# Kernel tuning notes

Measured on AMD Instinct MI355X. Metric: run time of the kernel, lower is better.

Reference implementation:

```python
import jax, jax.numpy as jnp
import numpy as np

DIM = 64
N_ENTITY = 1000000
N_RELATION = 32
L = 2
B = 4096
K = 64


def setup_inputs() -> dict:
    key = jax.random.key(0)
    ks = jax.random.split(key, 24)
    s = 0.05
    d = DIM
    inp = {
        "items": jax.random.randint(ks[0], (B,), 0, N_ENTITY),
        "heads": jax.random.randint(ks[1], (L, B, K), 0, N_ENTITY),
        "relations": jax.random.randint(ks[2], (L, B, K), 0, N_RELATION),
        "tails": jax.random.randint(ks[3], (L, B, K), 0, N_ENTITY),
        # learned parameters
        "embedding": jax.random.normal(ks[4], (N_ENTITY, d), jnp.float32) * s,
        "transformer": jax.random.normal(ks[5], (N_RELATION, d), jnp.float32) * s,
        "attn_w": jax.random.normal(ks[6], (1, 3 * d), jnp.float32) * s,
        "attn_b": jax.random.normal(ks[7], (1,), jnp.float32) * s,
        "W_ih": jax.random.normal(ks[8], (d, d), jnp.float32) * s,
        "W_hh": jax.random.normal(ks[9], (d, d), jnp.float32) * s,
        "b_ih": jax.random.normal(ks[10], (d,), jnp.float32) * s,
        "b_hh": jax.random.normal(ks[11], (d,), jnp.float32) * s,
        "l1_w": jax.random.normal(ks[12], (d, 2 * d), jnp.float32) * s,
        "l1_b": jax.random.normal(ks[13], (d,), jnp.float32) * s,
        "l2_w": jax.random.normal(ks[14], (d, d), jnp.float32) * s,
        "l2_b": jax.random.normal(ks[15], (d,), jnp.float32) * s,
        "l3_w": jax.random.normal(ks[16], (d, d), jnp.float32) * s,
        "l3_b": jax.random.normal(ks[17], (d,), jnp.float32) * s,
        "lin_w": jax.random.normal(ks[18], (1, 2 * d), jnp.float32) * s,
        "lin_b": jax.random.normal(ks[19], (1,), jnp.float32) * s,
    }
    return inp


def _ncfg_forward(embedding, transformer, attn_w, attn_b, W_ih, W_hh, b_ih, b_hh,
                  l1_w, l1_b, l2_w, l2_b, l3_w, l3_b, lin_w, lin_b,
                  items, heads, relations, tails):
    o_sum = jnp.zeros((B, DIM), embedding.dtype)
    for l in range(L):
        h = embedding[heads[l]]          # [B, K, d]
        r = transformer[relations[l]]    # [B, K, d]
        tl = embedding[tails[l]]         # [B, K, d]
        hRt = jnp.concatenate([h, r, tl], axis=-1)                  # [B, K, 3d]
        pi = jax.nn.sigmoid(hRt @ attn_w.T + attn_b)                # [B, K, 1]
        pi = jax.nn.softmax(pi, axis=1)                             # softmax over neighbors
        # 2-step tanh RNN over seq (head, tail), h0 = 0
        h1 = jnp.tanh(h @ W_ih.T + b_ih + b_hh)                     # [B, K, d]
        h2 = jnp.tanh(tl @ W_ih.T + b_ih + h1 @ W_hh.T + b_hh)      # [B, K, d]
        o_sum = o_sum + (pi * h2).sum(axis=1)                       # [B, d]
    user_emb = o_sum
    item_emb = embedding[items]                                     # [B, d]
    # NCF head (dropout in eval mode = identity)
    ui = jnp.concatenate([user_emb, item_emb], axis=-1)             # [B, 2d]
    y = jax.nn.relu(ui @ l1_w.T + l1_b)
    y = jax.nn.relu(y @ l2_w.T + l2_b)
    y1 = jax.nn.sigmoid(y @ l3_w.T + l3_b)
    y2 = user_emb * item_emb
    out = jax.nn.sigmoid(jnp.concatenate([y1, y2], axis=-1) @ lin_w.T + lin_b)
    return out[:, 0]  # squeeze -> [B]


def reference(items, heads, relations, tails, embedding, transformer, attn_w, attn_b,
              W_ih, W_hh, b_ih, b_hh, l1_w, l1_b, l2_w, l2_b, l3_w, l3_b, lin_w, lin_b):
    return _ncfg_forward(embedding, transformer, attn_w, attn_b, W_ih, W_hh, b_ih, b_hh,
                         l1_w, l1_b, l2_w, l2_b, l3_w, l3_b, lin_w, lin_b,
                         items, heads, relations, tails)
```

## Files before the change

### kernel.cpp

```cpp
#include <hip/hip_runtime.h>
#include <hip/hip_bf16.h>
#include <cstdint>
#include <cstddef>

#define B_SZ 4096

typedef __attribute__((ext_vector_type(4))) float f32x4;
typedef __attribute__((ext_vector_type(8))) short sv8;
typedef __attribute__((ext_vector_type(8))) __bf16 bfv8;

__device__ __align__(16) short g_wf[2][8][64][8];
__device__ __align__(16) short g_af[2][2][64][8];
__device__ float g_bsum[64];
__device__ float g_reldot[32];

static __device__ __forceinline__ short f2bf(float x) {
  union { float f; unsigned u; } v; v.f = x;
  unsigned r = v.u + 0x7fffu + ((v.u >> 16) & 1u);
  return (short)(r >> 16);
}

static __device__ __forceinline__ f32x4 MFMA(sv8 a, sv8 b, f32x4 c) {
  return __builtin_amdgcn_mfma_f32_16x16x32_bf16(
      __builtin_bit_cast(bfv8, a), __builtin_bit_cast(bfv8, b), c, 0, 0, 0);
}

static __device__ __forceinline__ float fast_sigmoid(float x) {
  return __builtin_amdgcn_rcpf(1.f + __expf(-x));
}
static __device__ __forceinline__ float fast_tanh(float x) {
  const float e = __expf(2.f * x);
  return 1.f - 2.f * __builtin_amdgcn_rcpf(e + 1.f);
}
static __device__ __forceinline__ sv8 pack8(f32x4 a, f32x4 b) {
  sv8 f;
  f[0] = f2bf(a.x); f[1] = f2bf(a.y); f[2] = f2bf(a.z); f[3] = f2bf(a.w);
  f[4] = f2bf(b.x); f[5] = f2bf(b.y); f[6] = f2bf(b.z); f[7] = f2bf(b.w);
  return f;
}

__global__ __launch_bounds__(256) void ncfg_prep(
    const float* __restrict__ W_ih, const float* __restrict__ W_hh,
    const float* __restrict__ b_ih, const float* __restrict__ b_hh,
    const float* __restrict__ trf, const float* __restrict__ attn_w) {
  const int t = threadIdx.x;
  for (int q = t; q < 1024; q += 256) {
    const int m = q >> 9, f = (q >> 6) & 7, ln = q & 63;
    const int nt = f >> 1, kh = f & 1, fr = ln & 15, fg = ln >> 4;
    const float* W = m ? W_hh : W_ih;
    const float* src = W + (nt * 16 + fr) * 64 + kh * 32 + fg * 8;
    short* dst = &g_wf[m][f][ln][0];
    #pragma unroll
    for (int j = 0; j < 8; ++j) dst[j] = f2bf(src[j]);
  }
  {
    const int a = t >> 7, kh = (t >> 6) & 1, ln = t & 63;
    const int n = ln & 15, kf = ln >> 4;
    short* dst = &g_af[a][kh][ln][0];
    #pragma unroll
    for (int j = 0; j < 8; ++j)
      dst[j] = (n == 0) ? f2bf(attn_w[a * 128 + kh * 32 + kf * 8 + j]) : (short)0;
  }
  if (t < 64) g_bsum[t] = b_ih[t] + b_hh[t];
  if (t < 32) {
    float s = 0.f;
    #pragma unroll 8
    for (int c = 0; c < 64; ++c) s += trf[t * 64 + c] * attn_w[64 + c];
    g_reldot[t] = s;
  }
}

__global__ __launch_bounds__(256, 3) void ncfg_neigh(
    const int* __restrict__ heads, const int* __restrict__ rels,
    const int* __restrict__ tails, const float* __restrict__ emb,
    const float* __restrict__ attn_b, float* __restrict__ opart) {
  const int t = threadIdx.x;
  const int lane = t & 63;
  const int w = t >> 6;
  const int fr = lane & 15;
  const int fg = lane >> 4;
  const int c0 = fg * 8;

  __shared__ __align__(16) short h1s[4][16 * 72];
  __shared__ float ow[4][64];
  __shared__ float sew[4];

  const size_t ibase = (size_t)blockIdx.x * 64;

  const int hi = heads[ibase + (w << 4) + fr];
  const int ti = tails[ibase + (w << 4) + fr];
  const int ri = rels[ibase + (w << 4) + fr];

  const float* hr = emb + (size_t)hi * 64;
  const float* tr = emb + (size_t)ti * 64;
  const f32x4 h0 = *(const f32x4*)(hr + c0);
  const f32x4 h1 = *(const f32x4*)(hr + c0 + 4);
  const f32x4 h2 = *(const f32x4*)(hr + 32 + c0);
  const f32x4 h3 = *(const f32x4*)(hr + 32 + c0 + 4);
  const f32x4 t0 = *(const f32x4*)(tr + c0);
  const f32x4 t1 = *(const f32x4*)(tr + c0 + 4);
  const f32x4 t2 = *(const f32x4*)(tr + 32 + c0);
  const f32x4 t3 = *(const f32x4*)(tr + 32 + c0 + 4);

  sv8 wih[8], abf[4];
  #pragma unroll
  for (int f = 0; f < 8; ++f) wih[f] = *(const sv8*)&g_wf[0][f][lane][0];
  abf[0] = *(const sv8*)&g_af[0][0][lane][0];
  abf[1] = *(const sv8*)&g_af[0][1][lane][0];
  abf[2] = *(const sv8*)&g_af[1][0][lane][0];
  abf[3] = *(const sv8*)&g_af[1][1][lane][0];
  float bsum[4];
  #pragma unroll
  for (int nt = 0; nt < 4; ++nt) bsum[nt] = g_bsum[nt * 16 + fr];
  const float ab0 = attn_b[0];

  const sv8 ha0 = pack8(h0, h1), ha1 = pack8(h2, h3);
  const sv8 ta0 = pack8(t0, t1), ta1 = pack8(t2, t3);

  const f32x4 zz = {0.f, 0.f, 0.f, 0.f};

  f32x4 accl = zz;
  accl = MFMA(ha0, abf[0], accl);
  accl = MFMA(ha1, abf[1], accl);
  accl = MFMA(ta0, abf[2], accl);
  accl = MFMA(ta1, abf[3], accl);

  f32x4 ev;
  #pragma unroll
  for (int r = 0; r < 4; ++r) {
    const float lg = __shfl(accl[r], fg << 4);
    const int rr = __shfl(ri, (fg << 2) + r);
    ev[r] = __expf(fast_sigmoid(lg + g_reldot[rr] + ab0));
  }
  float se = ev.x + ev.y + ev.z + ev.w;
  se += __shfl_xor(se, 16);
  se += __shfl_xor(se, 32);

  f32x4 acc[4] = {zz, zz, zz, zz};
  #pragma unroll
  for (int nt = 0; nt < 4; ++nt) acc[nt] = MFMA(ha0, wih[nt * 2], acc[nt]);
  #pragma unroll
  for (int nt = 0; nt < 4; ++nt) acc[nt] = MFMA(ha1, wih[nt * 2 + 1], acc[nt]);

  sv8 whh[8];
  #pragma unroll
  for (int f = 0; f < 8; ++f) whh[f] = *(const sv8*)&g_wf[1][f][lane][0];

  #pragma unroll
  for (int nt = 0; nt < 4; ++nt)
    #pragma unroll
    for (int r = 0; r < 4; ++r)
      h1s[w][((fg << 2) + r) * 72 + nt * 16 + fr] =
          f2bf(fast_tanh(acc[nt][r] + bsum[nt]));

  f32x4 acc2[4] = {zz, zz, zz, zz};
  #pragma unroll
  for (int nt = 0; nt < 4; ++nt) acc2[nt] = MFMA(ta0, wih[nt * 2], acc2[nt]);
  #pragma unroll
  for (int nt = 0; nt < 4; ++nt) acc2[nt] = MFMA(ta1, wih[nt * 2 + 1], acc2[nt]);
  const sv8 a1 = *(const sv8*)&h1s[w][fr * 72 + c0];
  const sv8 a2 = *(const sv8*)&h1s[w][fr * 72 + 32 + c0];
  #pragma unroll
  for (int nt = 0; nt < 4; ++nt) acc2[nt] = MFMA(a1, whh[nt * 2], acc2[nt]);
  #pragma unroll
  for (int nt = 0; nt < 4; ++nt) acc2[nt] = MFMA(a2, whh[nt * 2 + 1], acc2[nt]);

  #pragma unroll
  for (int nt = 0; nt < 4; ++nt) {
    float s = ev.x * fast_tanh(acc2[nt][0] + bsum[nt]) +
              ev.y * fast_tanh(acc2[nt][1] + bsum[nt]) +
              ev.z * fast_tanh(acc2[nt][2] + bsum[nt]) +
              ev.w * fast_tanh(acc2[nt][3] + bsum[nt]);
    s += __shfl_xor(s, 16);
    s += __shfl_xor(s, 32);
    if (fg == 0) ow[w][nt * 16 + fr] = s;
  }
  if (lane == 0) sew[w] = se;

  __syncthreads();

  if (w == 0) {
    const float o = ow[0][lane] + ow[1][lane] + ow[2][lane] + ow[3][lane];
    const float st = sew[0] + sew[1] + sew[2] + sew[3];
    opart[ibase + lane] = o * __builtin_amdgcn_rcpf(st);
  }
}

__global__ __launch_bounds__(256) void ncfg_head(
    const float* __restrict__ opart, const float* __restrict__ emb,
    const int* __restrict__ items, const float* __restrict__ l1_w,
    const float* __restrict__ l1_b, const float* __restrict__ l2_w,
    const float* __restrict__ l2_b, const float* __restrict__ l3_w,
    const float* __restrict__ l3_b, const float* __restrict__ lin_w,
    const float* __restrict__ lin_b, float* __restrict__ out) {
  const int wv = threadIdx.x >> 6;
  const int i = threadIdx.x & 63;
  const int b = blockIdx.x * 4 + wv;

  __shared__ float ui[4][128];
  __shared__ float yy[4][64];

  const float ue = opart[(size_t)b * 64 + i] +
                   opart[((size_t)B_SZ + b) * 64 + i];
  const float ie = emb[(size_t)items[b] * 64 + i];
  ui[wv][i] = ue;
  ui[wv][64 + i] = ie;
  __syncthreads();

  float acc = l1_b[i];
  {
    const float* wr = l1_w + i * 128;
    #pragma unroll
    for (int j = 0; j < 128; j += 4) {
      const f32x4 wvv = *(const f32x4*)(wr + j);
      const f32x4 uv = *(const f32x4*)&ui[wv][j];
      acc += wvv.x * uv.x + wvv.y * uv.y + wvv.z * uv.z + wvv.w * uv.w;
    }
  }
  float y = fmaxf(acc, 0.f);
  yy[wv][i] = y;
  __syncthreads();

  acc = l2_b[i];
  {
    const float* wr = l2_w + i * 64;
    #pragma unroll
    for (int j = 0; j < 64; j += 4) {
      const f32x4 wvv = *(const f32x4*)(wr + j);
      const f32x4 uv = *(const f32x4*)&yy[wv][j];
      acc += wvv.x * uv.x + wvv.y * uv.y + wvv.z * uv.z + wvv.w * uv.w;
    }
  }
  y = fmaxf(acc, 0.f);
  __syncthreads();
  yy[wv][i] = y;
  __syncthreads();

  acc = l3_b[i];
  {
    const float* wr = l3_w + i * 64;
    #pragma unroll
    for (int j = 0; j < 64; j += 4) {
      const f32x4 wvv = *(const f32x4*)(wr + j);
      const f32x4 uv = *(const f32x4*)&yy[wv][j];
      acc += wvv.x * uv.x + wvv.y * uv.y + wvv.z * uv.z + wvv.w * uv.w;
    }
  }
  const float y1 = fast_sigmoid(acc);
  const float y2 = ue * ie;

  float part = y1 * lin_w[i] + y2 * lin_w[64 + i];
  #pragma unroll
  for (int m = 1; m < 64; m <<= 1) part += __shfl_xor(part, m);
  if (i == 0) out[b] = fast_sigmoid(part + lin_b[0]);
}

extern "C" void kernel_launch(void* const* d_in, const int* in_sizes, int n_in,
                              void* d_out, int out_size, void* d_ws,
                              size_t ws_size, hipStream_t stream) {
  (void)in_sizes; (void)n_in; (void)out_size; (void)ws_size;
  const int* items = (const int*)d_in[0];
  const int* heads = (const int*)d_in[1];
  const int* rels = (const int*)d_in[2];
  const int* tails = (const int*)d_in[3];
  const float* emb = (const float*)d_in[4];
  const float* trf = (const float*)d_in[5];
  const float* attn_w = (const float*)d_in[6];
  const float* attn_b = (const float*)d_in[7];
  const float* W_ih = (const float*)d_in[8];
  const float* W_hh = (const float*)d_in[9];
  const float* b_ih = (const float*)d_in[10];
  const float* b_hh = (const float*)d_in[11];
  const float* l1_w = (const float*)d_in[12];
  const float* l1_b = (const float*)d_in[13];
  const float* l2_w = (const float*)d_in[14];
  const float* l2_b = (const float*)d_in[15];
  const float* l3_w = (const float*)d_in[16];
  const float* l3_b = (const float*)d_in[17];
  const float* lin_w = (const float*)d_in[18];
  const float* lin_b = (const float*)d_in[19];
  float* out = (float*)d_out;
  float* opart = (float*)d_ws;

  ncfg_prep<<<dim3(1), dim3(256), 0, stream>>>(W_ih, W_hh, b_ih, b_hh, trf,
                                               attn_w);
  ncfg_neigh<<<dim3(2 * B_SZ), dim3(256), 0, stream>>>(
      heads, rels, tails, emb, attn_b, opart);
  ncfg_head<<<dim3(B_SZ / 4), dim3(256), 0, stream>>>(
      opart, emb, items, l1_w, l1_b, l2_w, l2_b, l3_w, l3_b, lin_w, lin_b,
      out);
}
```

Before: 95.69 us.

## Process a whole item per wave with LDS-staged weights and prefetched gathers

Each wave now handles all 64 neighbours of one (layer, batch) item in four chunks of 16, instead of each block splitting one item across four waves. Weight fragments are staged once per block into LDS rather than held in registers from global memory. The next chunk's embedding rows are prefetched while the current chunk computes. The per-item reduction stays within the wave, so the cross-wave shared-memory reduction and end barrier go away, the grid shrinks by 4x, and the occupancy hint rises to 4. The costs are extra LDS reads for every MFMA operand, a barrier after staging, and more serial work per wave, which means fewer waves in flight to hide gather latency.

```diff
diff --git a/kernel.cpp b/kernel.cpp
--- a/kernel.cpp
+++ b/kernel.cpp
@@ -70,7 +70,7 @@
   }
 }
 
-__global__ __launch_bounds__(256, 3) void ncfg_neigh(
+__global__ __launch_bounds__(256, 4) void ncfg_neigh(
     const int* __restrict__ heads, const int* __restrict__ rels,
     const int* __restrict__ tails, const float* __restrict__ emb,
     const float* __restrict__ attn_b, float* __restrict__ opart) {
@@ -81,109 +81,133 @@
   const int fg = lane >> 4;
   const int c0 = fg * 8;
 
+  __shared__ __align__(16) short wlds[2][8][64][8];
+  __shared__ __align__(16) short alds[2][2][64][8];
+  __shared__ float rlds[32];
   __shared__ __align__(16) short h1s[4][16 * 72];
-  __shared__ float ow[4][64];
-  __shared__ float sew[4];
-
-  const size_t ibase = (size_t)blockIdx.x * 64;
-
-  const int hi = heads[ibase + (w << 4) + fr];
-  const int ti = tails[ibase + (w << 4) + fr];
-  const int ri = rels[ibase + (w << 4) + fr];
-
-  const float* hr = emb + (size_t)hi * 64;
-  const float* tr = emb + (size_t)ti * 64;
-  const f32x4 h0 = *(const f32x4*)(hr + c0);
-  const f32x4 h1 = *(const f32x4*)(hr + c0 + 4);
-  const f32x4 h2 = *(const f32x4*)(hr + 32 + c0);
-  const f32x4 h3 = *(const f32x4*)(hr + 32 + c0 + 4);
-  const f32x4 t0 = *(const f32x4*)(tr + c0);
-  const f32x4 t1 = *(const f32x4*)(tr + c0 + 4);
-  const f32x4 t2 = *(const f32x4*)(tr + 32 + c0);
-  const f32x4 t3 = *(const f32x4*)(tr + 32 + c0 + 4);
-
-  sv8 wih[8], abf[4];
-  #pragma unroll
-  for (int f = 0; f < 8; ++f) wih[f] = *(const sv8*)&g_wf[0][f][lane][0];
-  abf[0] = *(const sv8*)&g_af[0][0][lane][0];
-  abf[1] = *(const sv8*)&g_af[0][1][lane][0];
-  abf[2] = *(const sv8*)&g_af[1][0][lane][0];
-  abf[3] = *(const sv8*)&g_af[1][1][lane][0];
+
+  const int item = blockIdx.x * 4 + w;
+  const size_t ibase = (size_t)item * 64;
+
+  int hiA[4], tiA[4], riA[4];
+  #pragma unroll
+  for (int c = 0; c < 4; ++c) {
+    hiA[c] = heads[ibase + c * 16 + fr];
+    tiA[c] = tails[ibase + c * 16 + fr];
+    riA[c] = rels[ibase + c * 16 + fr];
+  }
   float bsum[4];
   #pragma unroll
   for (int nt = 0; nt < 4; ++nt) bsum[nt] = g_bsum[nt * 16 + fr];
   const float ab0 = attn_b[0];
 
-  const sv8 ha0 = pack8(h0, h1), ha1 = pack8(h2, h3);
-  const sv8 ta0 = pack8(t0, t1), ta1 = pack8(t2, t3);
+  {
+    const f32x4* s1 = (const f32x4*)&g_wf[0][0][0][0];
+    f32x4* d1 = (f32x4*)&wlds[0][0][0][0];
+    #pragma unroll
+    for (int i = 0; i < 4; ++i) d1[t + i * 256] = s1[t + i * 256];
+    const f32x4* s2 = (const f32x4*)&g_af[0][0][0][0];
+    ((f32x4*)&alds[0][0][0][0])[t] = s2[t];
+    if (t < 8) ((f32x4*)rlds)[t] = ((const f32x4*)g_reldot)[t];
+  }
+  __syncthreads();
+
+  f32x4 gh0, gh1, gh2, gh3, gt0, gt1, gt2, gt3;
+#define LOADG(cc)                                                     \
+  {                                                                   \
+    const float* hr_ = emb + (size_t)hiA[cc] * 64;                    \
+    const float* tr_ = emb + (size_t)tiA[cc] * 64;                    \
+    gh0 = *(const f32x4*)(hr_ + c0);                                  \
+    gh1 = *(const f32x4*)(hr_ + c0 + 4);                              \
+    gh2 = *(const f32x4*)(hr_ + 32 + c0);                             \
+    gh3 = *(const f32x4*)(hr_ + 32 + c0 + 4);                         \
+    gt0 = *(const f32x4*)(tr_ + c0);                                  \
+    gt1 = *(const f32x4*)(tr_ + c0 + 4);                              \
+    gt2 = *(const f32x4*)(tr_ + 32 + c0);                             \
+    gt3 = *(const f32x4*)(tr_ + 32 + c0 + 4);                         \
+  }
+
+  LOADG(0);
 
   const f32x4 zz = {0.f, 0.f, 0.f, 0.f};
-
-  f32x4 accl = zz;
-  accl = MFMA(ha0, abf[0], accl);
-  accl = MFMA(ha1, abf[1], accl);
-  accl = MFMA(ta0, abf[2], accl);
-  accl = MFMA(ta1, abf[3], accl);
-
-  f32x4 ev;
-  #pragma unroll
-  for (int r = 0; r < 4; ++r) {
-    const float lg = __shfl(accl[r], fg << 4);
-    const int rr = __shfl(ri, (fg << 2) + r);
-    ev[r] = __expf(fast_sigmoid(lg + g_reldot[rr] + ab0));
-  }
-  float se = ev.x + ev.y + ev.z + ev.w;
+  float o4[4] = {0.f, 0.f, 0.f, 0.f};
+  float se = 0.f;
+
+  #pragma unroll
+  for (int c = 0; c < 4; ++c) {
+    const sv8 ha0 = pack8(gh0, gh1), ha1 = pack8(gh2, gh3);
+    const sv8 ta0 = pack8(gt0, gt1), ta1 = pack8(gt2, gt3);
+    if (c < 3) LOADG(c + 1);
+
+    f32x4 accl = zz;
+    accl = MFMA(ha0, *(const sv8*)&alds[0][0][lane][0], accl);
+    accl = MFMA(ha1, *(const sv8*)&alds[0][1][lane][0], accl);
+    accl = MFMA(ta0, *(const sv8*)&alds[1][0][lane][0], accl);
+    accl = MFMA(ta1, *(const sv8*)&alds[1][1][lane][0], accl);
+
+    f32x4 ev;
+    #pragma unroll
+    for (int r = 0; r < 4; ++r) {
+      const float lg = __shfl(accl[r], fg << 4);
+      const int rr = __shfl(riA[c], (fg << 2) + r);
+      ev[r] = __expf(fast_sigmoid(lg + rlds[rr] + ab0));
+    }
+    se += ev.x + ev.y + ev.z + ev.w;
+
+    f32x4 acc[4] = {zz, zz, zz, zz};
+    #pragma unroll
+    for (int nt = 0; nt < 4; ++nt)
+      acc[nt] = MFMA(ha0, *(const sv8*)&wlds[0][nt * 2][lane][0], acc[nt]);
+    #pragma unroll
+    for (int nt = 0; nt < 4; ++nt)
+      acc[nt] = MFMA(ha1, *(const sv8*)&wlds[0][nt * 2 + 1][lane][0], acc[nt]);
+    #pragma unroll
+    for (int nt = 0; nt < 4; ++nt)
+      #pragma unroll
+      for (int r = 0; r < 4; ++r)
+        h1s[w][((fg << 2) + r) * 72 + nt * 16 + fr] =
+            f2bf(fast_tanh(acc[nt][r] + bsum[nt]));
+
+    f32x4 acc2[4] = {zz, zz, zz, zz};
+    #pragma unroll
+    for (int nt = 0; nt < 4; ++nt)
+      acc2[nt] = MFMA(ta0, *(const sv8*)&wlds[0][nt * 2][lane][0], acc2[nt]);
+    #pragma unroll
+    for (int nt = 0; nt < 4; ++nt)
+      acc2[nt] = MFMA(ta1, *(const sv8*)&wlds[0][nt * 2 + 1][lane][0], acc2[nt]);
+    const sv8 a1 = *(const sv8*)&h1s[w][fr * 72 + c0];
+    const sv8 a2 = *(const sv8*)&h1s[w][fr * 72 + 32 + c0];
+    #pragma unroll
+    for (int nt = 0; nt < 4; ++nt)
+      acc2[nt] = MFMA(a1, *(const sv8*)&wlds[1][nt * 2][lane][0], acc2[nt]);
+    #pragma unroll
+    for (int nt = 0; nt < 4; ++nt)
+      acc2[nt] = MFMA(a2, *(const sv8*)&wlds[1][nt * 2 + 1][lane][0], acc2[nt]);
+
+    #pragma unroll
+    for (int nt = 0; nt < 4; ++nt)
+      o4[nt] += ev.x * fast_tanh(acc2[nt][0] + bsum[nt]) +
+                ev.y * fast_tanh(acc2[nt][1] + bsum[nt]) +
+                ev.z * fast_tanh(acc2[nt][2] + bsum[nt]) +
+                ev.w * fast_tanh(acc2[nt][3] + bsum[nt]);
+  }
+#undef LOADG
+
+  #pragma unroll
+  for (int nt = 0; nt < 4; ++nt) {
+    o4[nt] += __shfl_xor(o4[nt], 16);
+    o4[nt] += __shfl_xor(o4[nt], 32);
+  }
   se += __shfl_xor(se, 16);
   se += __shfl_xor(se, 32);
-
-  f32x4 acc[4] = {zz, zz, zz, zz};
-  #pragma unroll
-  for (int nt = 0; nt < 4; ++nt) acc[nt] = MFMA(ha0, wih[nt * 2], acc[nt]);
-  #pragma unroll
-  for (int nt = 0; nt < 4; ++nt) acc[nt] = MFMA(ha1, wih[nt * 2 + 1], acc[nt]);
-
-  sv8 whh[8];
-  #pragma unroll
-  for (int f = 0; f < 8; ++f) whh[f] = *(const sv8*)&g_wf[1][f][lane][0];
-
-  #pragma unroll
-  for (int nt = 0; nt < 4; ++nt)
-    #pragma unroll
-    for (int r = 0; r < 4; ++r)
-      h1s[w][((fg << 2) + r) * 72 + nt * 16 + fr] =
-          f2bf(fast_tanh(acc[nt][r] + bsum[nt]));
-
-  f32x4 acc2[4] = {zz, zz, zz, zz};
-  #pragma unroll
-  for (int nt = 0; nt < 4; ++nt) acc2[nt] = MFMA(ta0, wih[nt * 2], acc2[nt]);
-  #pragma unroll
-  for (int nt = 0; nt < 4; ++nt) acc2[nt] = MFMA(ta1, wih[nt * 2 + 1], acc2[nt]);
-  const sv8 a1 = *(const sv8*)&h1s[w][fr * 72 + c0];
-  const sv8 a2 = *(const sv8*)&h1s[w][fr * 72 + 32 + c0];
-  #pragma unroll
-  for (int nt = 0; nt < 4; ++nt) acc2[nt] = MFMA(a1, whh[nt * 2], acc2[nt]);
-  #pragma unroll
-  for (int nt = 0; nt < 4; ++nt) acc2[nt] = MFMA(a2, whh[nt * 2 + 1], acc2[nt]);
-
-  #pragma unroll
-  for (int nt = 0; nt < 4; ++nt) {
-    float s = ev.x * fast_tanh(acc2[nt][0] + bsum[nt]) +
-              ev.y * fast_tanh(acc2[nt][1] + bsum[nt]) +
-              ev.z * fast_tanh(acc2[nt][2] + bsum[nt]) +
-              ev.w * fast_tanh(acc2[nt][3] + bsum[nt]);
-    s += __shfl_xor(s, 16);
-    s += __shfl_xor(s, 32);
-    if (fg == 0) ow[w][nt * 16 + fr] = s;
-  }
-  if (lane == 0) sew[w] = se;
-
-  __syncthreads();
-
-  if (w == 0) {
-    const float o = ow[0][lane] + ow[1][lane] + ow[2][lane] + ow[3][lane];
-    const float st = sew[0] + sew[1] + sew[2] + sew[3];
-    opart[ibase + lane] = o * __builtin_amdgcn_rcpf(st);
-  }
+  const float inv = __builtin_amdgcn_rcpf(se);
+
+  const float r0 = __shfl(o4[0], fr);
+  const float r1 = __shfl(o4[1], fr);
+  const float r2 = __shfl(o4[2], fr);
+  const float r3 = __shfl(o4[3], fr);
+  const float oval = (fg == 0) ? r0 : (fg == 1) ? r1 : (fg == 2) ? r2 : r3;
+  opart[ibase + lane] = oval * inv;
 }
 
 __global__ __launch_bounds__(256) void ncfg_head(
@@ -284,7 +308,7 @@
 
   ncfg_prep<<<dim3(1), dim3(256), 0, stream>>>(W_ih, W_hh, b_ih, b_hh, trf,
                                                attn_w);
-  ncfg_neigh<<<dim3(2 * B_SZ), dim3(256), 0, stream>>>(
+  ncfg_neigh<<<dim3(2 * B_SZ / 4), dim3(256), 0, stream>>>(
       heads, rels, tails, emb, attn_b, opart);
   ncfg_head<<<dim3(B_SZ / 4), dim3(256), 0, stream>>>(
       opart, emb, items, l1_w, l1_b, l2_w, l2_b, l3_w, l3_b, lin_w, lin_b,
```

Result: slower. 147.9 us (+54.6%).

## Stage RNN and attention weights in LDS per block, raise occupancy target

Applied to the files above, without the earlier changes.

Each block now copies the pre-swizzled bf16 weight fragments, attention fragments and relation dot table from global memory into shared memory, and the MFMAs read their B operands from LDS instead of keeping 20 sv8 fragments in registers. This lowers VGPR pressure so the launch bound can move from 3 to 4 waves per SIMD, aiming to hide the latency of the random embedding gathers. The change also swaps the manual float-to-bf16 rounding for the intrinsic conversion and moves the softmax-denominator shuffles later. In exchange every block pays about 17KB of extra LDS traffic plus an added barrier, and the larger LDS footprint may itself cap occupancy.

```diff
diff --git a/kernel.cpp b/kernel.cpp
--- a/kernel.cpp
+++ b/kernel.cpp
@@ -19,6 +19,9 @@
   unsigned r = v.u + 0x7fffu + ((v.u >> 16) & 1u);
   return (short)(r >> 16);
 }
+static __device__ __forceinline__ short f2bfc(float x) {
+  return (short)__builtin_bit_cast(unsigned short, __float2bfloat16(x));
+}
 
 static __device__ __forceinline__ f32x4 MFMA(sv8 a, sv8 b, f32x4 c) {
   return __builtin_amdgcn_mfma_f32_16x16x32_bf16(
@@ -34,8 +37,8 @@
 }
 static __device__ __forceinline__ sv8 pack8(f32x4 a, f32x4 b) {
   sv8 f;
-  f[0] = f2bf(a.x); f[1] = f2bf(a.y); f[2] = f2bf(a.z); f[3] = f2bf(a.w);
-  f[4] = f2bf(b.x); f[5] = f2bf(b.y); f[6] = f2bf(b.z); f[7] = f2bf(b.w);
+  f[0] = f2bfc(a.x); f[1] = f2bfc(a.y); f[2] = f2bfc(a.z); f[3] = f2bfc(a.w);
+  f[4] = f2bfc(b.x); f[5] = f2bfc(b.y); f[6] = f2bfc(b.z); f[7] = f2bfc(b.w);
   return f;
 }
 
@@ -70,7 +73,7 @@
   }
 }
 
-__global__ __launch_bounds__(256, 3) void ncfg_neigh(
+__global__ __launch_bounds__(256, 4) void ncfg_neigh(
     const int* __restrict__ heads, const int* __restrict__ rels,
     const int* __restrict__ tails, const float* __restrict__ emb,
     const float* __restrict__ attn_b, float* __restrict__ opart) {
@@ -81,6 +84,9 @@
   const int fg = lane >> 4;
   const int c0 = fg * 8;
 
+  __shared__ __align__(16) short wlds[2][8][64][8];
+  __shared__ __align__(16) short alds[2][2][64][8];
+  __shared__ float rlds[32];
   __shared__ __align__(16) short h1s[4][16 * 72];
   __shared__ float ow[4][64];
   __shared__ float sew[4];
@@ -90,6 +96,21 @@
   const int hi = heads[ibase + (w << 4) + fr];
   const int ti = tails[ibase + (w << 4) + fr];
   const int ri = rels[ibase + (w << 4) + fr];
+
+  {
+    const f32x4* s1 = (const f32x4*)&g_wf[0][0][0][0];
+    f32x4* d1 = (f32x4*)&wlds[0][0][0][0];
+    #pragma unroll
+    for (int i = 0; i < 4; ++i) d1[t + i * 256] = s1[t + i * 256];
+    const f32x4* s2 = (const f32x4*)&g_af[0][0][0][0];
+    ((f32x4*)&alds[0][0][0][0])[t] = s2[t];
+    if (t < 8) ((f32x4*)rlds)[t] = ((const f32x4*)g_reldot)[t];
+  }
+
+  float bsum[4];
+  #pragma unroll
+  for (int nt = 0; nt < 4; ++nt) bsum[nt] = g_bsum[nt * 16 + fr];
+  const float ab0 = attn_b[0];
 
   const float* hr = emb + (size_t)hi * 64;
   const float* tr = emb + (size_t)ti * 64;
@@ -102,17 +123,7 @@
   const f32x4 t2 = *(const f32x4*)(tr + 32 + c0);
   const f32x4 t3 = *(const f32x4*)(tr + 32 + c0 + 4);
 
-  sv8 wih[8], abf[4];
-  #pragma unroll
-  for (int f = 0; f < 8; ++f) wih[f] = *(const sv8*)&g_wf[0][f][lane][0];
-  abf[0] = *(const sv8*)&g_af[0][0][lane][0];
-  abf[1] = *(const sv8*)&g_af[0][1][lane][0];
-  abf[2] = *(const sv8*)&g_af[1][0][lane][0];
-  abf[3] = *(const sv8*)&g_af[1][1][lane][0];
-  float bsum[4];
-  #pragma unroll
-  for (int nt = 0; nt < 4; ++nt) bsum[nt] = g_bsum[nt * 16 + fr];
-  const float ab0 = attn_b[0];
+  __syncthreads();
 
   const sv8 ha0 = pack8(h0, h1), ha1 = pack8(h2, h3);
   const sv8 ta0 = pack8(t0, t1), ta1 = pack8(t2, t3);
@@ -120,50 +131,49 @@
   const f32x4 zz = {0.f, 0.f, 0.f, 0.f};
 
   f32x4 accl = zz;
-  accl = MFMA(ha0, abf[0], accl);
-  accl = MFMA(ha1, abf[1], accl);
-  accl = MFMA(ta0, abf[2], accl);
-  accl = MFMA(ta1, abf[3], accl);
+  accl = MFMA(ha0, *(const sv8*)&alds[0][0][lane][0], accl);
+  accl = MFMA(ha1, *(const sv8*)&alds[0][1][lane][0], accl);
+  accl = MFMA(ta0, *(const sv8*)&alds[1][0][lane][0], accl);
+  accl = MFMA(ta1, *(const sv8*)&alds[1][1][lane][0], accl);
 
   f32x4 ev;
   #pragma unroll
   for (int r = 0; r < 4; ++r) {
     const float lg = __shfl(accl[r], fg << 4);
     const int rr = __shfl(ri, (fg << 2) + r);
-    ev[r] = __expf(fast_sigmoid(lg + g_reldot[rr] + ab0));
+    ev[r] = __expf(fast_sigmoid(lg + rlds[rr] + ab0));
   }
   float se = ev.x + ev.y + ev.z + ev.w;
-  se += __shfl_xor(se, 16);
-  se += __shfl_xor(se, 32);
 
   f32x4 acc[4] = {zz, zz, zz, zz};
   #pragma unroll
-  for (int nt = 0; nt < 4; ++nt) acc[nt] = MFMA(ha0, wih[nt * 2], acc[nt]);
-  #pragma unroll
-  for (int nt = 0; nt < 4; ++nt) acc[nt] = MFMA(ha1, wih[nt * 2 + 1], acc[nt]);
-
-  sv8 whh[8];
-  #pragma unroll
-  for (int f = 0; f < 8; ++f) whh[f] = *(const sv8*)&g_wf[1][f][lane][0];
-
+  for (int nt = 0; nt < 4; ++nt)
+    acc[nt] = MFMA(ha0, *(const sv8*)&wlds[0][nt * 2][lane][0], acc[nt]);
+  #pragma unroll
+  for (int nt = 0; nt < 4; ++nt)
+    acc[nt] = MFMA(ha1, *(const sv8*)&wlds[0][nt * 2 + 1][lane][0], acc[nt]);
   #pragma unroll
   for (int nt = 0; nt < 4; ++nt)
     #pragma unroll
     for (int r = 0; r < 4; ++r)
       h1s[w][((fg << 2) + r) * 72 + nt * 16 + fr] =
-          f2bf(fast_tanh(acc[nt][r] + bsum[nt]));
+          f2bfc(fast_tanh(acc[nt][r] + bsum[nt]));
 
   f32x4 acc2[4] = {zz, zz, zz, zz};
   #pragma unroll
-  for (int nt = 0; nt < 4; ++nt) acc2[nt] = MFMA(ta0, wih[nt * 2], acc2[nt]);
-  #pragma unroll
-  for (int nt = 0; nt < 4; ++nt) acc2[nt] = MFMA(ta1, wih[nt * 2 + 1], acc2[nt]);
+  for (int nt = 0; nt < 4; ++nt)
+    acc2[nt] = MFMA(ta0, *(const sv8*)&wlds[0][nt * 2][lane][0], acc2[nt]);
+  #pragma unroll
+  for (int nt = 0; nt < 4; ++nt)
+    acc2[nt] = MFMA(ta1, *(const sv8*)&wlds[0][nt * 2 + 1][lane][0], acc2[nt]);
   const sv8 a1 = *(const sv8*)&h1s[w][fr * 72 + c0];
   const sv8 a2 = *(const sv8*)&h1s[w][fr * 72 + 32 + c0];
   #pragma unroll
-  for (int nt = 0; nt < 4; ++nt) acc2[nt] = MFMA(a1, whh[nt * 2], acc2[nt]);
-  #pragma unroll
-  for (int nt = 0; nt < 4; ++nt) acc2[nt] = MFMA(a2, whh[nt * 2 + 1], acc2[nt]);
+  for (int nt = 0; nt < 4; ++nt)
+    acc2[nt] = MFMA(a1, *(const sv8*)&wlds[1][nt * 2][lane][0], acc2[nt]);
+  #pragma unroll
+  for (int nt = 0; nt < 4; ++nt)
+    acc2[nt] = MFMA(a2, *(const sv8*)&wlds[1][nt * 2 + 1][lane][0], acc2[nt]);
 
   #pragma unroll
   for (int nt = 0; nt < 4; ++nt) {
@@ -175,6 +185,8 @@
     s += __shfl_xor(s, 32);
     if (fg == 0) ow[w][nt * 16 + fr] = s;
   }
+  se += __shfl_xor(se, 16);
+  se += __shfl_xor(se, 32);
   if (lane == 0) sew[w] = se;
 
   __syncthreads();
```

After: 85.18 us. 11.0% less time.
